# Optimization experiments

Hardware: AMD Instinct MI355X
Metric: run time of the kernel (lower is better)

The kernel has to match this reference:

```python
import jax, jax.numpy as jnp
import numpy as np

LATENT_SHAPES = [(192, 2, 2), (48, 4, 4), (24, 8, 8), (12, 16, 16), (6, 32, 32)]
B = 4          # batch
M = 32         # num_bases
HT, WT = 32, 32  # target spatial size = spatial size of z[-1] = (H/2, W/2)
EPS = 1e-3
CT = sum(s[0] for s in LATENT_SHAPES)  # 282


def _forward_fft(zs):
    # strided zero-insertion upsample of each latent to (HT, WT), concat channels, 2D FFT
    ups = []
    for zi in zs:
        b, c, h, w = zi.shape
        rh, rw = HT // h, WT // w
        u = jnp.zeros((b, c, HT, WT), zi.dtype).at[..., ::rh, ::rw].set(zi)
        ups.append(u)
    z = jnp.concatenate(ups, axis=1)            # (B, CT, HT, WT)
    return jnp.fft.fftn(z, axes=(-2, -1))       # complex64


def _inverse_fft(v_fft):
    # inverse FFT, take real part, split channels per level, strided downsample
    v = jnp.fft.ifftn(v_fft, axes=(-2, -1)).real  # (B, M, CT, HT, WT)
    splits = np.cumsum([s[0] for s in LATENT_SHAPES])[:-1]
    parts = jnp.split(v, splits, axis=-3)
    out = []
    for vi, (c, h, w) in zip(parts, LATENT_SHAPES):
        rh, rw = HT // h, WT // w
        out.append(vi[..., ::rh, ::rw])           # (B, M, c, h, w)
    return out


def _vector_field(zs, L, lam):
    z_fft = _forward_fft(zs)
    La = (L - jnp.swapaxes(L, -1, -2)).astype(jnp.complex64)        # antisymmetric (M, CT, CT)
    lam_a = (lam - jnp.roll(jnp.flip(lam, (1, 2)), (1, 1), axis=(1, 2))) * 1j  # (M, HT, WT) imaginary
    v_fft = jnp.einsum('mcd,bchw->bmdhw', La, z_fft)                 # (B, M, CT, HT, WT) complex
    v_fft = v_fft * lam_a[None, :, None, :, :]
    return _inverse_fft(v_fft)


def _log_prob(ws, zs, L, lam):
    S_ww = sum(jnp.einsum('bchw,bchw->b', wi, wi) for wi in ws)      # (B,)
    v = _vector_field(zs, L, lam)
    S_zz = sum(jnp.einsum('bnchw,bmchw->bnm', vi, vi) for vi in v)   # (B, M, M)
    S_zw = sum(jnp.einsum('bnchw,bchw->bn', vi, wi) for vi, wi in zip(v, ws))  # (B, M)
    var = jnp.maximum(jnp.mean(jnp.diagonal(S_zz, axis1=-2, axis2=-1), -1), 1e-6)
    std = jnp.sqrt(var)
    S_zz = S_zz / var[:, None, None]
    S_zw = S_zw / std[:, None]
    I = jnp.eye(M, dtype=S_zz.dtype)
    Mm = S_zz + EPS * I
    trace = EPS * S_ww + jnp.einsum('bn,bn->b', S_zw, S_zw)
    Lh = jnp.linalg.cholesky(Mm)
    logdet = 2.0 * jnp.sum(jnp.log(jnp.diagonal(Lh, axis1=-2, axis2=-1)), -1)
    return 0.5 * (logdet - trace)


def setup_inputs() -> dict:
    key = jax.random.key(0)
    ks = jax.random.split(key, 12)
    inp = {}
    for i, (c, h, w) in enumerate(LATENT_SHAPES):
        inp[f'z{i}'] = jax.random.normal(ks[i], (B, c, h, w), jnp.float32)
        inp[f'w{i}'] = jax.random.normal(ks[5 + i], (B, c, h, w), jnp.float32)
    inp['L'] = jax.random.normal(ks[10], (M, CT, CT), jnp.float32) * np.float32(1.0 / np.sqrt(CT))
    inp['lam'] = jax.random.normal(ks[11], (M, HT, WT), jnp.float32)
    return inp


def reference(z0, z1, z2, z3, z4, w0, w1, w2, w3, w4, L, lam):
    return _log_prob([w0, w1, w2, w3, w4], [z0, z1, z2, z3, z4], L, lam)
```

## Files before the change

kernel.cpp:

```cpp
#include <hip/hip_runtime.h>
#include <math.h>

#define NB 4
#define NM 32
#define CTOT 282
#define EPSV 1e-3f

__constant__ int g_cL[5]   = {192,48,24,12,6};
__constant__ int g_hL[5]   = {2,4,8,16,32};
__constant__ int g_coff[5] = {0,192,240,264,276};
__constant__ int g_zo[5]   = {0,768,1536,3072,6144};
__constant__ int g_po[4]   = {0,4,20,84};

__constant__ int t_lo[48] = {0,0,0,0,0,0,0,0,0,0,0,0,0,0,0,0,
                             0,0,0,0,0,0,0,0,0,0,0,0,0,0,0,0,
                             1,1,1,1,1,1,1,1, 2,2,2,2, 3,3, 4,4};
__constant__ int t_d0[48] = {0,6,12,18,24,30,36,42,48,54,60,66,72,78,84,90,
                             96,102,108,114,120,126,132,138,144,150,156,162,168,174,180,186,
                             192,198,204,210,216,222,228,234, 240,246,252,258, 264,270, 276,279};
__constant__ int t_nd[48] = {6,6,6,6,6,6,6,6,6,6,6,6,6,6,6,6,
                             6,6,6,6,6,6,6,6,6,6,6,6,6,6,6,6,
                             6,6,6,6,6,6,6,6, 6,6,6,6, 6,6, 3,3};

__constant__ int dft_l[30]  = {0,0,0, 1,1,1, 2,2,2,2,2,2,
                               3,3,3,3,3,3,3,3,3,3,3,3, 4,4,4,4,4,4};
__constant__ int dft_c0[30] = {0,64,128, 0,16,32, 0,4,8,12,16,20,
                               0,1,2,3,4,5,6,7,8,9,10,11, 0,1,2,3,4,5};
__constant__ int dft_nc[30] = {64,64,64, 16,16,16, 4,4,4,4,4,4,
                               1,1,1,1,1,1,1,1,1,1,1,1, 1,1,1,1,1,1};

#define N_LA     (NM*CTOT*CTOT)
#define OFF_LAT  0
#define OFF_ZRE  (OFF_LAT + N_LA)
#define OFF_ZIM  (OFF_ZRE + NB*12288)
#define OFF_WRE  (OFF_ZIM + NB*12288)
#define OFF_WIM  (OFF_WRE + NB*12288)
#define OFF_LAM  (OFF_WIM + NB*12288)
#define OFF_LAMF (OFF_LAM + NM*1024)
#define OFF_UR   (OFF_LAMF + NM*340)
#define OFF_UI   (OFF_UR + NB*NM*2720)
#define OFF_VRE  (OFF_UI + NB*NM*2720)
#define OFF_VIM  (OFF_VRE + NB*NM*12288)
#define OFF_SZZ  (OFF_VIM + NB*NM*12288)
#define OFF_SZW  (OFF_SZZ + NB*NM*NM)
#define OFF_SWW  (OFF_SZW + NB*NM)

#define PRE_LAT   (NM*81)
#define PRE_LAMF  (PRE_LAT + NM)
#define PRE_DFT   (PRE_LAMF + 2*NB*30)
#define PRE_SWW   (PRE_DFT + NB)
#define PRE_ZERO  (PRE_SWW + 17)

__global__ void __launch_bounds__(256) k_pre(
    const float* z0,const float* z1,const float* z2,const float* z3,const float* z4,
    const float* w0,const float* w1,const float* w2,const float* w3,const float* w4,
    const float* __restrict__ L, const float* __restrict__ lam, float* __restrict__ ws){
  __shared__ float shm[3136];
  int bid = blockIdx.x, t = threadIdx.x;
  if (bid < PRE_LAT){
    float* A  = shm;
    float* Bt = shm + 1056;
    int m = bid/81; int tl = bid%81;
    int d0 = (tl/9)*32, c0 = (tl%9)*32;
    const float* Lm = L + (size_t)m*CTOT*CTOT;
    for (int i=t;i<1024;i+=256){
      int r=i>>5, c=i&31;
      A[r*33+c]  = (c0+r<CTOT && d0+c<CTOT) ? Lm[(c0+r)*CTOT + d0+c] : 0.f;
      Bt[r*33+c] = (d0+r<CTOT && c0+c<CTOT) ? Lm[(d0+r)*CTOT + c0+c] : 0.f;
    }
    __syncthreads();
    float* out = ws + OFF_LAT + (size_t)m*CTOT*CTOT;
    for (int i=t;i<1024;i+=256){
      int r=i>>5, c=i&31;
      if (d0+r<CTOT && c0+c<CTOT)
        out[(size_t)(d0+r)*CTOT + c0+c] = A[c*33+r] - Bt[r*33+c];
    }
    return;
  }
  if (bid < PRE_LAMF){
    float* sA = shm;
    float* f3 = shm + 1024;
    float* f2 = shm + 1280;
    float* f1 = shm + 1344;
    int m = bid - PRE_LAT;
    for (int k=t;k<1024;k+=256){
      int ky=k>>5, kx=k&31;
      int nk = (((32-ky)&31)<<5) | ((32-kx)&31);
      float v = lam[(m<<10)+k] - lam[(m<<10)+nk];
      sA[k]=v;
      ws[OFF_LAM+(m<<10)+k]=v;
    }
    __syncthreads();
    { int s=t; int ky=s>>4, kx=s&15;
      float v = sA[(ky<<5)+kx]+sA[((ky+16)<<5)+kx]+sA[(ky<<5)+kx+16]+sA[((ky+16)<<5)+kx+16];
      f3[s]=v; ws[OFF_LAMF+m*340+84+s]=v; }
    __syncthreads();
    if (t<64){ int ky=t>>3, kx=t&7;
      float v = f3[(ky<<4)+kx]+f3[((ky+8)<<4)+kx]+f3[(ky<<4)+kx+8]+f3[((ky+8)<<4)+kx+8];
      f2[t]=v; ws[OFF_LAMF+m*340+20+t]=v; }
    __syncthreads();
    if (t<16){ int ky=t>>2, kx=t&3;
      float v = f2[(ky<<3)+kx]+f2[((ky+4)<<3)+kx]+f2[(ky<<3)+kx+4]+f2[((ky+4)<<3)+kx+4];
      f1[t]=v; ws[OFF_LAMF+m*340+4+t]=v; }
    __syncthreads();
    if (t<4){ int ky=t>>1, kx=t&1;
      float v = f1[(ky<<2)+kx]+f1[((ky+2)<<2)+kx]+f1[(ky<<2)+kx+2]+f1[((ky+2)<<2)+kx+2];
      ws[OFF_LAMF+m*340+t]=v; }
    return;
  }
  if (bid < PRE_DFT){
    float* sIn = shm;
    float* s1r = shm + 1024;
    float* s1i = shm + 2048;
    float* lc  = shm + 3072;
    float* lsn = shm + 3104;
    int i0 = bid - PRE_LAMF;
    int which = i0 / (NB*30);
    int rem = i0 % (NB*30);
    int b = rem / 30, j = rem % 30;
    int l = dft_l[j], c0 = dft_c0[j], nc = dft_nc[j];
    int h = g_hL[l], n = h*h;
    int elems = nc*n;
    const float* src;
    switch (which*5 + l){
      case 0: src=z0; break; case 1: src=z1; break; case 2: src=z2; break;
      case 3: src=z3; break; case 4: src=z4; break;
      case 5: src=w0; break; case 6: src=w1; break; case 7: src=w2; break;
      case 8: src=w3; break; default: src=w4; break;
    }
    for (int i=t;i<elems;i+=256) sIn[i] = src[(b*g_cL[l] + c0)*n + i];
    if (t<h){
      float ang = -6.2831853071795864f * (float)t / (float)h;
      lc[t] = cosf(ang); lsn[t] = sinf(ang);
    }
    __syncthreads();
    for (int p=t;p<elems;p+=256){
      int p2=p%n, cc=p/n;
      int y=p2/h, kx=p2-y*h;
      float re=0.f, im=0.f;
      for (int x=0;x<h;x++){
        int id = (kx*x)%h;
        float v = sIn[cc*n + y*h + x];
        re += v*lc[id]; im += v*lsn[id];
      }
      s1r[p]=re; s1i[p]=im;
    }
    __syncthreads();
    float scale = which ? 1.0f/(float)h : 1.0f;
    bool zt = (which==0 && l<4);
    float* outR = ws + (which?OFF_WRE:OFF_ZRE) + b*12288 + g_zo[l];
    float* outI = ws + (which?OFF_WIM:OFF_ZIM) + b*12288 + g_zo[l];
    for (int p=t;p<elems;p+=256){
      int p2=p%n, cc=p/n;
      int ky=p2/h, kx=p2-(p2/h)*h;
      float re=0.f, im=0.f;
      for (int y=0;y<h;y++){
        int id=(ky*y)%h;
        float c=lc[id], s=lsn[id];
        float ar=s1r[cc*n + y*h + kx], ai=s1i[cc*n + y*h + kx];
        re += ar*c - ai*s;
        im += ar*s + ai*c;
      }
      int o = zt ? (p2*g_cL[l] + c0 + cc) : ((c0+cc)*n + p2);
      outR[o]=re*scale; outI[o]=im*scale;
    }
    return;
  }
  if (bid < PRE_SWW){
    float* red = shm;
    int b = bid - PRE_DFT;
    const float* ptr[5] = {w0,w1,w2,w3,w4};
    float s = 0.f;
    for (int l=0;l<5;l++){
      int sz = g_cL[l]*g_hL[l]*g_hL[l];
      const float* p = ptr[l] + b*sz;
      for (int i=t;i<sz;i+=256){ float v=p[i]; s += v*v; }
    }
    red[t]=s; __syncthreads();
    for (int o=128;o>0;o>>=1){ if (t<o) red[t]+=red[t+o]; __syncthreads(); }
    if (t==0) ws[OFF_SWW + b] = red[0];
    return;
  }
  int i = (bid - PRE_SWW)*256 + t;
  if (i < NB*NM*NM + NB*NM) ws[OFF_SZZ + i] = 0.f;
}

__global__ void k_u(float* __restrict__ ws){
  __shared__ float pr[1024], pi[1024], q3r[256],q3i[256],q2r[64],q2i[64],q1r[16],q1i[16];
  int bid = blockIdx.x, t = threadIdx.x;
  int c = bid%6; int m = (bid/6)%NM; int b = bid/(6*NM);
  const float* la = ws+OFF_LAM+(m<<10);
  const float* zr = ws+OFF_ZRE+b*12288+6144+(c<<10);
  const float* zi = ws+OFF_ZIM+b*12288+6144+(c<<10);
  for (int k=t;k<1024;k+=256){ float f=la[k]; pr[k]=f*zr[k]; pi[k]=f*zi[k]; }
  __syncthreads();
  size_t base = (size_t)(b*NM+m)*2720;
  float* UR = ws+OFF_UR+base; float* UI = ws+OFF_UI+base;
  { int s=t; int ky=s>>4, kx=s&15;
    float r = pr[(ky<<5)+kx]+pr[((ky+16)<<5)+kx]+pr[(ky<<5)+kx+16]+pr[((ky+16)<<5)+kx+16];
    float ii= pi[(ky<<5)+kx]+pi[((ky+16)<<5)+kx]+pi[(ky<<5)+kx+16]+pi[((ky+16)<<5)+kx+16];
    q3r[s]=r; q3i[s]=ii; UR[(84+s)*8+c]=r; UI[(84+s)*8+c]=ii; }
  __syncthreads();
  if (t<64){ int ky=t>>3, kx=t&7;
    float r = q3r[(ky<<4)+kx]+q3r[((ky+8)<<4)+kx]+q3r[(ky<<4)+kx+8]+q3r[((ky+8)<<4)+kx+8];
    float ii= q3i[(ky<<4)+kx]+q3i[((ky+8)<<4)+kx]+q3i[(ky<<4)+kx+8]+q3i[((ky+8)<<4)+kx+8];
    q2r[t]=r; q2i[t]=ii; UR[(20+t)*8+c]=r; UI[(20+t)*8+c]=ii; }
  __syncthreads();
  if (t<16){ int ky=t>>2, kx=t&3;
    float r = q2r[(ky<<3)+kx]+q2r[((ky+4)<<3)+kx]+q2r[(ky<<3)+kx+4]+q2r[((ky+4)<<3)+kx+4];
    float ii= q2i[(ky<<3)+kx]+q2i[((ky+4)<<3)+kx]+q2i[(ky<<3)+kx+4]+q2i[((ky+4)<<3)+kx+4];
    q1r[t]=r; q1i[t]=ii; UR[(4+t)*8+c]=r; UI[(4+t)*8+c]=ii; }
  __syncthreads();
  if (t<4){ int ky=t>>1, kx=t&1;
    float r = q1r[(ky<<2)+kx]+q1r[((ky+2)<<2)+kx]+q1r[(ky<<2)+kx+2]+q1r[((ky+2)<<2)+kx+2];
    float ii= q1i[(ky<<2)+kx]+q1i[((ky+2)<<2)+kx]+q1i[(ky<<2)+kx+2]+q1i[((ky+2)<<2)+kx+2];
    UR[t*8+c]=r; UI[t*8+c]=ii; }
}

__global__ void __launch_bounds__(256) k_fold(float* __restrict__ ws){
  __shared__ float smem[6160];
  float* pre   = smem;
  float* pim   = smem + 2040;
  float* sLa   = smem + 4080;
  float* c64r  = smem + 4080;
  float* c64i  = smem + 4464;
  float* c16r  = smem + 4848;
  float* c16i  = smem + 4944;
  float* c4r   = smem + 5040;
  float* c4i   = smem + 5064;
  float* lamf  = smem + 5784;
  float* ssla  = smem + 6124;

  int t = threadIdx.x, bid = blockIdx.x;
  int m    = bid / (NB*48);
  int rem  = bid % (NB*48);
  int b    = rem / 48;
  int tile = rem % 48;
  int lo = t_lo[tile], d0 = t_d0[tile], nd = t_nd[tile];
  int ho = g_hL[lo];
  int nbins = ho*ho;
  const float* zreb = ws + OFF_ZRE + b*12288;
  const float* zimb = ws + OFF_ZIM + b*12288;
  const float* latm = ws + OFF_LAT + (size_t)m*CTOT*CTOT;

  for (int i=t;i<340;i+=256) lamf[i] = ws[OFF_LAMF + m*340 + i];
  for (int i=t;i<nd*282;i+=256){ int d=i/282, c=i-d*282; sLa[d*284+c] = latm[(size_t)(d0+d)*CTOT + c]; }
  if (t<nd*6){ int d=t/6, c=t-d*6; ssla[t] = latm[(size_t)(d0+d)*CTOT + 276 + c]; }

  int lA, kkA, c0A, offP; bool wrt;
  if (t<64){ lA=0; kkA=t&3; c0A=(t>>2)*12; offP=0; wrt=(t<4); }
  else if (t<128){ int i=t-64; lA=1; kkA=i&15; c0A=(i>>4)*12; offP=4; wrt=(i<16); }
  else { int i=t-128; lA=2; kkA=i>>1; c0A=(i&1)*12; offP=20; wrt=((i&1)==0); }
  float zAr[12], zAi[12], zBr[12], zBi[12];
  {
    int oA = g_zo[lA] + kkA*g_cL[lA] + c0A;
    const float4* zr4 = (const float4*)(zreb + oA);
    const float4* zi4 = (const float4*)(zimb + oA);
    float4 x0=zr4[0], x1=zr4[1], x2=zr4[2];
    float4 y0=zi4[0], y1=zi4[1], y2=zi4[2];
    zAr[0]=x0.x;zAr[1]=x0.y;zAr[2]=x0.z;zAr[3]=x0.w;zAr[4]=x1.x;zAr[5]=x1.y;zAr[6]=x1.z;zAr[7]=x1.w;zAr[8]=x2.x;zAr[9]=x2.y;zAr[10]=x2.z;zAr[11]=x2.w;
    zAi[0]=y0.x;zAi[1]=y0.y;zAi[2]=y0.z;zAi[3]=y0.w;zAi[4]=y1.x;zAi[5]=y1.y;zAi[6]=y1.z;zAi[7]=y1.w;zAi[8]=y2.x;zAi[9]=y2.y;zAi[10]=y2.z;zAi[11]=y2.w;
    int oB = 3072 + t*12;
    const float4* zr3 = (const float4*)(zreb + oB);
    const float4* zi3 = (const float4*)(zimb + oB);
    float4 p0=zr3[0], p1=zr3[1], p2=zr3[2];
    float4 q0=zi3[0], q1=zi3[1], q2=zi3[2];
    zBr[0]=p0.x;zBr[1]=p0.y;zBr[2]=p0.z;zBr[3]=p0.w;zBr[4]=p1.x;zBr[5]=p1.y;zBr[6]=p1.z;zBr[7]=p1.w;zBr[8]=p2.x;zBr[9]=p2.y;zBr[10]=p2.z;zBr[11]=p2.w;
    zBi[0]=q0.x;zBi[1]=q0.y;zBi[2]=q0.z;zBi[3]=q0.w;zBi[4]=q1.x;zBi[5]=q1.y;zBi[6]=q1.z;zBi[7]=q1.w;zBi[8]=q2.x;zBi[9]=q2.y;zBi[10]=q2.z;zBi[11]=q2.w;
  }
  __syncthreads();

  int offA = g_coff[lA] + c0A;
  for (int d=0; d<nd; d++){
    const float4* laA = (const float4*)(sLa + d*284 + offA);
    const float4* laB = (const float4*)(sLa + d*284 + 264);
    float4 a0=laA[0], a1=laA[1], a2=laA[2];
    float4 b0=laB[0], b1=laB[1], b2=laB[2];
    float av[12] = {a0.x,a0.y,a0.z,a0.w, a1.x,a1.y,a1.z,a1.w, a2.x,a2.y,a2.z,a2.w};
    float bv[12] = {b0.x,b0.y,b0.z,b0.w, b1.x,b1.y,b1.z,b1.w, b2.x,b2.y,b2.z,b2.w};
    float prA=0.f, piA=0.f, prB=0.f, piB=0.f;
    #pragma unroll
    for (int c=0;c<12;c++){ prA+=av[c]*zAr[c]; piA+=av[c]*zAi[c]; }
    #pragma unroll
    for (int c=0;c<12;c++){ prB+=bv[c]*zBr[c]; piB+=bv[c]*zBi[c]; }
    if (t<64){
      prA += __shfl_xor(prA, 4);  piA += __shfl_xor(piA, 4);
      prA += __shfl_xor(prA, 8);  piA += __shfl_xor(piA, 8);
      prA += __shfl_xor(prA,16);  piA += __shfl_xor(piA,16);
      prA += __shfl_xor(prA,32);  piA += __shfl_xor(piA,32);
    } else if (t<128){
      prA += __shfl_xor(prA,16);  piA += __shfl_xor(piA,16);
      prA += __shfl_xor(prA,32);  piA += __shfl_xor(piA,32);
    } else {
      prA += __shfl_xor(prA, 1);  piA += __shfl_xor(piA, 1);
    }
    if (wrt){ pre[d*340+offP+kkA]=prA; pim[d*340+offP+kkA]=piA; }
    pre[d*340+84+t]=prB; pim[d*340+84+t]=piB;
  }
  __syncthreads();

  float sc = (float)ho/1024.f;
  if (lo==4){
    int dlb = d0 - 276;
    const float* lamA = ws + OFF_LAM + (m<<10);
    float* vRb = ws + OFF_VRE + (size_t)(b*NM+m)*12288 + 6144 + (dlb<<10);
    float* vIb = ws + OFF_VIM + (size_t)(b*NM+m)*12288 + 6144 + (dlb<<10);
    const float* z4r = zreb + 6144;
    const float* z4i = zimb + 6144;
    for (int q=t; q<1024; q+=256){
      int ky=q>>5, kx=q&31;
      int a0=((ky&1)<<1)|(kx&1);
      int a1=4+(((ky&3)<<2)|(kx&3));
      int a2=20+(((ky&7)<<3)|(kx&7));
      int a3=84+(((ky&15)<<4)|(kx&15));
      float zr_[6], zi_[6];
      #pragma unroll
      for (int c=0;c<6;c++){ zr_[c]=z4r[(c<<10)+q]; zi_[c]=z4i[(c<<10)+q]; }
      float lm = lamA[q]*sc;
      for (int d=0; d<nd; d++){
        const float* pd = pre + d*340; const float* qd = pim + d*340;
        float Br = pd[a0]+pd[a1]+pd[a2]+pd[a3];
        float Bi = qd[a0]+qd[a1]+qd[a2]+qd[a3];
        #pragma unroll
        for (int c=0;c<6;c++){ float a=ssla[d*6+c]; Br+=a*zr_[c]; Bi+=a*zi_[c]; }
        vRb[(d<<10)+q] = -lm*Bi;
        vIb[(d<<10)+q] =  lm*Br;
      }
    }
    return;
  }

  if (lo<3){
    for (int idx=t; idx<nd*64; idx+=256){
      int d=idx>>6, k2=idx&63, ky=k2>>3, kx=k2&7;
      const float* pd = pre + d*340 + 84; const float* qd = pim + d*340 + 84;
      float r=0.f, ii=0.f;
      #pragma unroll
      for (int jy=0;jy<2;jy++)
        #pragma unroll
        for (int jx=0;jx<2;jx++){
          int a = ((ky+8*jy)<<4) | (kx+8*jx);
          float f = lamf[84+a];
          r += f*pd[a]; ii += f*qd[a];
        }
      if (lo<2){ float f=lamf[20+k2]; r+=f*pre[d*340+20+k2]; ii+=f*pim[d*340+20+k2]; }
      c64r[idx]=r; c64i[idx]=ii;
    }
  }
  __syncthreads();
  if (lo<2){
    for (int idx=t; idx<nd*16; idx+=256){
      int d=idx>>4, k2=idx&15, ky=k2>>2, kx=k2&3, base=d<<6;
      float r = c64r[base+(ky<<3)+kx]+c64r[base+((ky+4)<<3)+kx]+c64r[base+(ky<<3)+kx+4]+c64r[base+((ky+4)<<3)+kx+4];
      float ii= c64i[base+(ky<<3)+kx]+c64i[base+((ky+4)<<3)+kx]+c64i[base+(ky<<3)+kx+4]+c64i[base+((ky+4)<<3)+kx+4];
      if (lo<1){ float f=lamf[4+k2]; r+=f*pre[d*340+4+k2]; ii+=f*pim[d*340+4+k2]; }
      c16r[idx]=r; c16i[idx]=ii;
    }
  }
  __syncthreads();
  if (lo==0 && t<nd*4){
    int d=t>>2, k2=t&3, ky=k2>>1, kx=k2&1, base=d<<4;
    c4r[t]=c16r[base+(ky<<2)+kx]+c16r[base+((ky+2)<<2)+kx]+c16r[base+(ky<<2)+kx+2]+c16r[base+((ky+2)<<2)+kx+2];
    c4i[t]=c16i[base+(ky<<2)+kx]+c16i[base+((ky+2)<<2)+kx]+c16i[base+(ky<<2)+kx+2]+c16i[base+((ky+2)<<2)+kx+2];
  }
  __syncthreads();

  int dlb = d0 - g_coff[lo];
  float* vRb = ws + OFF_VRE + (size_t)(b*NM+m)*12288 + g_zo[lo];
  float* vIb = ws + OFF_VIM + (size_t)(b*NM+m)*12288 + g_zo[lo];
  const float* URg = ws + OFF_UR + (size_t)(b*NM+m)*2720;
  const float* UIg = ws + OFF_UI + (size_t)(b*NM+m)*2720;
  for (int idx=t; idx<nd*nbins; idx+=256){
    int d=idx/nbins, bin=idx-d*nbins;
    int ky=bin/ho, kx=bin-ky*ho;
    const float* pd = pre + d*340; const float* qd = pim + d*340;
    float Br = pd[((ky&1)<<1)|(kx&1)], Bi = qd[((ky&1)<<1)|(kx&1)];
    if (lo>=1){ int ix=4+(((ky&3)<<2)|(kx&3)); Br+=pd[ix]; Bi+=qd[ix]; }
    if (lo>=2){ int ix=20+(((ky&7)<<3)|(kx&7)); Br+=pd[ix]; Bi+=qd[ix]; }
    if (lo>=3){ int ix=84+(((ky&15)<<4)|(kx&15)); Br+=pd[ix]; Bi+=qd[ix]; }
    float lf = lamf[g_po[lo]+bin];
    float Vr = lf*Br, Vi = lf*Bi;
    if (lo==2){ Vr+=c64r[(d<<6)+bin]; Vi+=c64i[(d<<6)+bin]; }
    else if (lo==1){ Vr+=c16r[(d<<4)+bin]; Vi+=c16i[(d<<4)+bin]; }
    else if (lo==0){ Vr+=c4r[(d<<2)+bin]; Vi+=c4i[(d<<2)+bin]; }
    {
      int e = (g_po[lo]+bin)*8;
      const float4* ur4 = (const float4*)(URg + e);
      const float4* ui4 = (const float4*)(UIg + e);
      float4 u0=ur4[0], u1=ur4[1];
      float4 v0=ui4[0], v1=ui4[1];
      const float* sd = ssla + d*6;
      Vr += sd[0]*u0.x + sd[1]*u0.y + sd[2]*u0.z + sd[3]*u0.w + sd[4]*u1.x + sd[5]*u1.y;
      Vi += sd[0]*v0.x + sd[1]*v0.y + sd[2]*v0.z + sd[3]*v0.w + sd[4]*v1.x + sd[5]*v1.y;
    }
    int ob = (dlb+d)*nbins + bin;
    vRb[ob] = -sc*Vi;
    vIb[ob] =  sc*Vr;
  }
}

__global__ void __launch_bounds__(256) k_gram(float* __restrict__ ws){
  __shared__ float tile[32*132];
  __shared__ float wv[128];
  int t = threadIdx.x;
  int bid = blockIdx.x;
  int b = bid / 192, ch = bid % 192;
  int half = ch / 96;
  int k0 = (ch % 96) * 128;
  const float* V = ws + (half?OFF_VIM:OFF_VRE);
  const float* W = ws + (half?OFF_WIM:OFF_WRE) + b*12288 + k0;
  #pragma unroll
  for (int p=0;p<4;p++){
    int i4 = t + (p<<8);
    int row = i4 >> 5, c4 = i4 & 31;
    float4 v = *(const float4*)(V + (size_t)(b*NM+row)*12288 + k0 + (c4<<2));
    *(float4*)(tile + row*132 + (c4<<2)) = v;
  }
  if (t<128) wv[t] = W[t];
  __syncthreads();
  const float4* tf = (const float4*)tile;
  int n0 = t>>5, mm = t&31;
  float acc0=0.f, acc1=0.f, acc2=0.f, acc3=0.f;
  const float4* rm = tf + mm*33;
  const float4* r0 = tf + n0*33;
  const float4* r1 = tf + (n0+8)*33;
  const float4* r2 = tf + (n0+16)*33;
  const float4* r3 = tf + (n0+24)*33;
  for (int k4=0;k4<32;k4++){
    float4 vm = rm[k4];
    float4 v0 = r0[k4];
    float4 v1 = r1[k4];
    float4 v2 = r2[k4];
    float4 v3 = r3[k4];
    acc0 += v0.x*vm.x + v0.y*vm.y + v0.z*vm.z + v0.w*vm.w;
    acc1 += v1.x*vm.x + v1.y*vm.y + v1.z*vm.z + v1.w*vm.w;
    acc2 += v2.x*vm.x + v2.y*vm.y + v2.z*vm.z + v2.w*vm.w;
    acc3 += v3.x*vm.x + v3.y*vm.y + v3.z*vm.z + v3.w*vm.w;
  }
  float* szz = ws + OFF_SZZ + (b<<10);
  atomicAdd(&szz[(n0<<5) + mm], acc0);
  atomicAdd(&szz[((n0+8)<<5) + mm], acc1);
  atomicAdd(&szz[((n0+16)<<5) + mm], acc2);
  atomicAdd(&szz[((n0+24)<<5) + mm], acc3);
  if (t < 32){
    const float4* rn = tf + t*33;
    const float4* wf = (const float4*)wv;
    float acc=0.f;
    for (int k4=0;k4<32;k4++){
      float4 a = rn[k4]; float4 wq = wf[k4];
      acc += a.x*wq.x + a.y*wq.y + a.z*wq.z + a.w*wq.w;
    }
    atomicAdd(&ws[OFF_SZW + (b<<5) + t], acc);
  }
}

__global__ void k_final(float* __restrict__ ws, float* __restrict__ out){
  __shared__ float A[32][33];
  __shared__ float svar;
  int b = blockIdx.x, t = threadIdx.x;
  const float* szz = ws + OFF_SZZ + (b<<10);
  if (t==0){
    float s=0.f;
    for (int i=0;i<32;i++) s += szz[i*33];
    svar = fmaxf(s/32.0f, 1e-6f);
  }
  __syncthreads();
  float var = svar;
  for (int i=t;i<1024;i+=64){
    int r=i>>5, c=i&31;
    A[r][c] = szz[i]/var + ((r==c)?EPSV:0.0f);
  }
  __syncthreads();
  for (int j=0;j<32;j++){
    if (t==0) A[j][j] = sqrtf(A[j][j]);
    __syncthreads();
    if (t>j && t<32) A[t][j] /= A[j][j];
    __syncthreads();
    if (t>j && t<32){
      float lij = A[t][j];
      for (int k=j+1;k<=t;k++) A[t][k] -= lij*A[k][j];
    }
    __syncthreads();
  }
  if (t==0){
    float logdet=0.f;
    for (int j=0;j<32;j++) logdet += logf(A[j][j]);
    logdet *= 2.0f;
    const float* szw = ws + OFF_SZW + (b<<5);
    float s2=0.f;
    for (int n=0;n<32;n++) s2 += szw[n]*szw[n];
    float trace = EPSV*ws[OFF_SWW + b] + s2/var;
    out[b] = 0.5f*(logdet - trace);
  }
}

extern "C" void kernel_launch(void* const* d_in, const int* in_sizes, int n_in,
                              void* d_out, int out_size, void* d_ws, size_t ws_size,
                              hipStream_t stream){
  const float* z0 = (const float*)d_in[0];
  const float* w0 = (const float*)d_in[1];
  const float* z1 = (const float*)d_in[2];
  const float* w1 = (const float*)d_in[3];
  const float* z2 = (const float*)d_in[4];
  const float* w2 = (const float*)d_in[5];
  const float* z3 = (const float*)d_in[6];
  const float* w3 = (const float*)d_in[7];
  const float* z4 = (const float*)d_in[8];
  const float* w4 = (const float*)d_in[9];
  const float* L   = (const float*)d_in[10];
  const float* lam = (const float*)d_in[11];
  float* ws = (float*)d_ws;
  float* out = (float*)d_out;

  k_pre<<<PRE_ZERO, 256, 0, stream>>>(z0,z1,z2,z3,z4,w0,w1,w2,w3,w4, L, lam, ws);
  k_u<<<NB*NM*6, 256, 0, stream>>>(ws);
  k_fold<<<NB*NM*48, 256, 0, stream>>>(ws);
  k_gram<<<NB*192, 256, 0, stream>>>(ws);
  k_final<<<NB, 64, 0, stream>>>(ws, out);
}
```

Before: 208.5 us.

## Enlarge antisymmetrize tiles, pad DFT shared buffers, move z transpose into k_u

```diff
diff --git a/kernel.cpp b/kernel.cpp
--- a/kernel.cpp
+++ b/kernel.cpp
@@ -37,7 +37,9 @@
 #define OFF_WIM  (OFF_WRE + NB*12288)
 #define OFF_LAM  (OFF_WIM + NB*12288)
 #define OFF_LAMF (OFF_LAM + NM*1024)
-#define OFF_UR   (OFF_LAMF + NM*340)
+#define OFF_ZTR  (OFF_LAMF + NM*340)
+#define OFF_ZTI  (OFF_ZTR + NB*6144)
+#define OFF_UR   (OFF_ZTI + NB*6144)
 #define OFF_UI   (OFF_UR + NB*NM*2720)
 #define OFF_VRE  (OFF_UI + NB*NM*2720)
 #define OFF_VIM  (OFF_VRE + NB*NM*12288)
@@ -45,7 +47,7 @@
 #define OFF_SZW  (OFF_SZZ + NB*NM*NM)
 #define OFF_SWW  (OFF_SZW + NB*NM)
 
-#define PRE_LAT   (NM*81)
+#define PRE_LAT   (NM*25)
 #define PRE_LAMF  (PRE_LAT + NM)
 #define PRE_DFT   (PRE_LAMF + 2*NB*30)
 #define PRE_SWW   (PRE_DFT + NB)
@@ -55,25 +57,23 @@
     const float* z0,const float* z1,const float* z2,const float* z3,const float* z4,
     const float* w0,const float* w1,const float* w2,const float* w3,const float* w4,
     const float* __restrict__ L, const float* __restrict__ lam, float* __restrict__ ws){
-  __shared__ float shm[3136];
+  __shared__ float shm[4160];
   int bid = blockIdx.x, t = threadIdx.x;
   if (bid < PRE_LAT){
-    float* A  = shm;
-    float* Bt = shm + 1056;
-    int m = bid/81; int tl = bid%81;
-    int d0 = (tl/9)*32, c0 = (tl%9)*32;
+    int m = bid/25, tl = bid%25;
+    int d0 = (tl/5)*64, c0 = (tl%5)*64;
     const float* Lm = L + (size_t)m*CTOT*CTOT;
-    for (int i=t;i<1024;i+=256){
-      int r=i>>5, c=i&31;
-      A[r*33+c]  = (c0+r<CTOT && d0+c<CTOT) ? Lm[(c0+r)*CTOT + d0+c] : 0.f;
-      Bt[r*33+c] = (d0+r<CTOT && c0+c<CTOT) ? Lm[(d0+r)*CTOT + c0+c] : 0.f;
+    float* At = shm;
+    for (int i=t;i<4096;i+=256){
+      int r=i>>6, c=i&63;
+      At[r*65+c] = (c0+r<CTOT && d0+c<CTOT) ? Lm[(size_t)(c0+r)*CTOT + d0+c] : 0.f;
     }
     __syncthreads();
     float* out = ws + OFF_LAT + (size_t)m*CTOT*CTOT;
-    for (int i=t;i<1024;i+=256){
-      int r=i>>5, c=i&31;
+    for (int i=t;i<4096;i+=256){
+      int r=i>>6, c=i&63;
       if (d0+r<CTOT && c0+c<CTOT)
-        out[(size_t)(d0+r)*CTOT + c0+c] = A[c*33+r] - Bt[r*33+c];
+        out[(size_t)(d0+r)*CTOT + c0+c] = At[c*65+r] - Lm[(size_t)(d0+r)*CTOT + c0+c];
     }
     return;
   }
@@ -111,15 +111,17 @@
   if (bid < PRE_DFT){
     float* sIn = shm;
     float* s1r = shm + 1024;
-    float* s1i = shm + 2048;
-    float* lc  = shm + 3072;
-    float* lsn = shm + 3104;
+    float* s1i = shm + 2080;
+    float* lc  = shm + 3136;
+    float* lsn = shm + 3168;
     int i0 = bid - PRE_LAMF;
     int which = i0 / (NB*30);
     int rem = i0 % (NB*30);
     int b = rem / 30, j = rem % 30;
     int l = dft_l[j], c0 = dft_c0[j], nc = dft_nc[j];
     int h = g_hL[l], n = h*h;
+    int hp = h+1, n1 = h*hp;
+    int mult = 32/h;
     int elems = nc*n;
     const float* src;
     switch (which*5 + l){
@@ -129,8 +131,8 @@
       case 8: src=w3; break; default: src=w4; break;
     }
     for (int i=t;i<elems;i+=256) sIn[i] = src[(b*g_cL[l] + c0)*n + i];
-    if (t<h){
-      float ang = -6.2831853071795864f * (float)t / (float)h;
+    if (t<32){
+      float ang = -6.2831853071795864f * (float)t / 32.0f;
       lc[t] = cosf(ang); lsn[t] = sinf(ang);
     }
     __syncthreads();
@@ -139,30 +141,28 @@
       int y=p2/h, kx=p2-y*h;
       float re=0.f, im=0.f;
       for (int x=0;x<h;x++){
-        int id = (kx*x)%h;
+        int id = ((kx*x)%h)*mult;
         float v = sIn[cc*n + y*h + x];
         re += v*lc[id]; im += v*lsn[id];
       }
-      s1r[p]=re; s1i[p]=im;
+      s1r[cc*n1 + y*hp + kx]=re; s1i[cc*n1 + y*hp + kx]=im;
     }
     __syncthreads();
     float scale = which ? 1.0f/(float)h : 1.0f;
-    bool zt = (which==0 && l<4);
-    float* outR = ws + (which?OFF_WRE:OFF_ZRE) + b*12288 + g_zo[l];
-    float* outI = ws + (which?OFF_WIM:OFF_ZIM) + b*12288 + g_zo[l];
+    float* outR = ws + (which?OFF_WRE:OFF_ZRE) + b*12288 + g_zo[l] + c0*n;
+    float* outI = ws + (which?OFF_WIM:OFF_ZIM) + b*12288 + g_zo[l] + c0*n;
     for (int p=t;p<elems;p+=256){
       int p2=p%n, cc=p/n;
       int ky=p2/h, kx=p2-(p2/h)*h;
       float re=0.f, im=0.f;
       for (int y=0;y<h;y++){
-        int id=(ky*y)%h;
+        int id=((ky*y)%h)*mult;
         float c=lc[id], s=lsn[id];
-        float ar=s1r[cc*n + y*h + kx], ai=s1i[cc*n + y*h + kx];
+        float ar=s1r[cc*n1 + y*hp + kx], ai=s1i[cc*n1 + y*hp + kx];
         re += ar*c - ai*s;
         im += ar*s + ai*c;
       }
-      int o = zt ? (p2*g_cL[l] + c0 + cc) : ((c0+cc)*n + p2);
-      outR[o]=re*scale; outI[o]=im*scale;
+      outR[p]=re*scale; outI[p]=im*scale;
     }
     return;
   }
@@ -186,35 +186,60 @@
 }
 
 __global__ void k_u(float* __restrict__ ws){
-  __shared__ float pr[1024], pi[1024], q3r[256],q3i[256],q2r[64],q2i[64],q1r[16],q1i[16];
+  __shared__ float shm[6144];
   int bid = blockIdx.x, t = threadIdx.x;
-  int c = bid%6; int m = (bid/6)%NM; int b = bid/(6*NM);
-  const float* la = ws+OFF_LAM+(m<<10);
-  const float* zr = ws+OFF_ZRE+b*12288+6144+(c<<10);
-  const float* zi = ws+OFF_ZIM+b*12288+6144+(c<<10);
-  for (int k=t;k<1024;k+=256){ float f=la[k]; pr[k]=f*zr[k]; pi[k]=f*zi[k]; }
-  __syncthreads();
-  size_t base = (size_t)(b*NM+m)*2720;
-  float* UR = ws+OFF_UR+base; float* UI = ws+OFF_UI+base;
-  { int s=t; int ky=s>>4, kx=s&15;
-    float r = pr[(ky<<5)+kx]+pr[((ky+16)<<5)+kx]+pr[(ky<<5)+kx+16]+pr[((ky+16)<<5)+kx+16];
-    float ii= pi[(ky<<5)+kx]+pi[((ky+16)<<5)+kx]+pi[(ky<<5)+kx+16]+pi[((ky+16)<<5)+kx+16];
-    q3r[s]=r; q3i[s]=ii; UR[(84+s)*8+c]=r; UI[(84+s)*8+c]=ii; }
-  __syncthreads();
-  if (t<64){ int ky=t>>3, kx=t&7;
-    float r = q3r[(ky<<4)+kx]+q3r[((ky+8)<<4)+kx]+q3r[(ky<<4)+kx+8]+q3r[((ky+8)<<4)+kx+8];
-    float ii= q3i[(ky<<4)+kx]+q3i[((ky+8)<<4)+kx]+q3i[(ky<<4)+kx+8]+q3i[((ky+8)<<4)+kx+8];
-    q2r[t]=r; q2i[t]=ii; UR[(20+t)*8+c]=r; UI[(20+t)*8+c]=ii; }
-  __syncthreads();
-  if (t<16){ int ky=t>>2, kx=t&3;
-    float r = q2r[(ky<<3)+kx]+q2r[((ky+4)<<3)+kx]+q2r[(ky<<3)+kx+4]+q2r[((ky+4)<<3)+kx+4];
-    float ii= q2i[(ky<<3)+kx]+q2i[((ky+4)<<3)+kx]+q2i[(ky<<3)+kx+4]+q2i[((ky+4)<<3)+kx+4];
-    q1r[t]=r; q1i[t]=ii; UR[(4+t)*8+c]=r; UI[(4+t)*8+c]=ii; }
-  __syncthreads();
-  if (t<4){ int ky=t>>1, kx=t&1;
-    float r = q1r[(ky<<2)+kx]+q1r[((ky+2)<<2)+kx]+q1r[(ky<<2)+kx+2]+q1r[((ky+2)<<2)+kx+2];
-    float ii= q1i[(ky<<2)+kx]+q1i[((ky+2)<<2)+kx]+q1i[(ky<<2)+kx+2]+q1i[((ky+2)<<2)+kx+2];
-    UR[t*8+c]=r; UI[t*8+c]=ii; }
+  if (bid < NB*NM*6){
+    float* pr = shm;
+    float* pi = shm + 1024;
+    float* q3r= shm + 2048;
+    float* q3i= shm + 2304;
+    float* q2r= shm + 2560;
+    float* q2i= shm + 2624;
+    float* q1r= shm + 2688;
+    float* q1i= shm + 2704;
+    int c = bid%6; int m = (bid/6)%NM; int b = bid/(6*NM);
+    const float* la = ws+OFF_LAM+(m<<10);
+    const float* zr = ws+OFF_ZRE+b*12288+6144+(c<<10);
+    const float* zi = ws+OFF_ZIM+b*12288+6144+(c<<10);
+    for (int k=t;k<1024;k+=256){ float f=la[k]; pr[k]=f*zr[k]; pi[k]=f*zi[k]; }
+    __syncthreads();
+    size_t base = (size_t)(b*NM+m)*2720;
+    float* UR = ws+OFF_UR+base; float* UI = ws+OFF_UI+base;
+    { int s=t; int ky=s>>4, kx=s&15;
+      float r = pr[(ky<<5)+kx]+pr[((ky+16)<<5)+kx]+pr[(ky<<5)+kx+16]+pr[((ky+16)<<5)+kx+16];
+      float ii= pi[(ky<<5)+kx]+pi[((ky+16)<<5)+kx]+pi[(ky<<5)+kx+16]+pi[((ky+16)<<5)+kx+16];
+      q3r[s]=r; q3i[s]=ii; UR[(84+s)*8+c]=r; UI[(84+s)*8+c]=ii; }
+    __syncthreads();
+    if (t<64){ int ky=t>>3, kx=t&7;
+      float r = q3r[(ky<<4)+kx]+q3r[((ky+8)<<4)+kx]+q3r[(ky<<4)+kx+8]+q3r[((ky+8)<<4)+kx+8];
+      float ii= q3i[(ky<<4)+kx]+q3i[((ky+8)<<4)+kx]+q3i[(ky<<4)+kx+8]+q3i[((ky+8)<<4)+kx+8];
+      q2r[t]=r; q2i[t]=ii; UR[(20+t)*8+c]=r; UI[(20+t)*8+c]=ii; }
+    __syncthreads();
+    if (t<16){ int ky=t>>2, kx=t&3;
+      float r = q2r[(ky<<3)+kx]+q2r[((ky+4)<<3)+kx]+q2r[(ky<<3)+kx+4]+q2r[((ky+4)<<3)+kx+4];
+      float ii= q2i[(ky<<3)+kx]+q2i[((ky+4)<<3)+kx]+q2i[(ky<<3)+kx+4]+q2i[((ky+4)<<3)+kx+4];
+      q1r[t]=r; q1i[t]=ii; UR[(4+t)*8+c]=r; UI[(4+t)*8+c]=ii; }
+    __syncthreads();
+    if (t<4){ int ky=t>>1, kx=t&1;
+      float r = q1r[(ky<<2)+kx]+q1r[((ky+2)<<2)+kx]+q1r[(ky<<2)+kx+2]+q1r[((ky+2)<<2)+kx+2];
+      float ii= q1i[(ky<<2)+kx]+q1i[((ky+2)<<2)+kx]+q1i[(ky<<2)+kx+2]+q1i[((ky+2)<<2)+kx+2];
+      UR[t*8+c]=r; UI[t*8+c]=ii; }
+    return;
+  }
+  int tid = bid - NB*NM*6;
+  int b = tid>>1, ri = tid&1;
+  const float* src = ws + (ri?OFF_ZIM:OFF_ZRE) + b*12288;
+  float* dst = ws + (ri?OFF_ZTI:OFF_ZTR) + b*6144;
+  for (int i=t;i<6144;i+=256) shm[i]=src[i];
+  __syncthreads();
+  for (int q=t;q<6144;q+=256){
+    int s;
+    if (q<768){ int bin=q/192, c=q-bin*192; s=c*4+bin; }
+    else if (q<1536){ int q2=q-768; int bin=q2/48, c=q2-bin*48; s=768+c*16+bin; }
+    else if (q<3072){ int q2=q-1536; int bin=q2/24, c=q2-bin*24; s=1536+c*64+bin; }
+    else { int q2=q-3072; int bin=q2/12, c=q2-bin*12; s=3072+c*256+bin; }
+    dst[q]=shm[s];
+  }
 }
 
 __global__ void __launch_bounds__(256) k_fold(float* __restrict__ ws){
@@ -241,6 +266,8 @@
   int nbins = ho*ho;
   const float* zreb = ws + OFF_ZRE + b*12288;
   const float* zimb = ws + OFF_ZIM + b*12288;
+  const float* ztr  = ws + OFF_ZTR + b*6144;
+  const float* zti  = ws + OFF_ZTI + b*6144;
   const float* latm = ws + OFF_LAT + (size_t)m*CTOT*CTOT;
 
   for (int i=t;i<340;i+=256) lamf[i] = ws[OFF_LAMF + m*340 + i];
@@ -254,15 +281,15 @@
   float zAr[12], zAi[12], zBr[12], zBi[12];
   {
     int oA = g_zo[lA] + kkA*g_cL[lA] + c0A;
-    const float4* zr4 = (const float4*)(zreb + oA);
-    const float4* zi4 = (const float4*)(zimb + oA);
+    const float4* zr4 = (const float4*)(ztr + oA);
+    const float4* zi4 = (const float4*)(zti + oA);
     float4 x0=zr4[0], x1=zr4[1], x2=zr4[2];
     float4 y0=zi4[0], y1=zi4[1], y2=zi4[2];
     zAr[0]=x0.x;zAr[1]=x0.y;zAr[2]=x0.z;zAr[3]=x0.w;zAr[4]=x1.x;zAr[5]=x1.y;zAr[6]=x1.z;zAr[7]=x1.w;zAr[8]=x2.x;zAr[9]=x2.y;zAr[10]=x2.z;zAr[11]=x2.w;
     zAi[0]=y0.x;zAi[1]=y0.y;zAi[2]=y0.z;zAi[3]=y0.w;zAi[4]=y1.x;zAi[5]=y1.y;zAi[6]=y1.z;zAi[7]=y1.w;zAi[8]=y2.x;zAi[9]=y2.y;zAi[10]=y2.z;zAi[11]=y2.w;
     int oB = 3072 + t*12;
-    const float4* zr3 = (const float4*)(zreb + oB);
-    const float4* zi3 = (const float4*)(zimb + oB);
+    const float4* zr3 = (const float4*)(ztr + oB);
+    const float4* zi3 = (const float4*)(zti + oB);
     float4 p0=zr3[0], p1=zr3[1], p2=zr3[2];
     float4 q0=zi3[0], q1=zi3[1], q2=zi3[2];
     zBr[0]=p0.x;zBr[1]=p0.y;zBr[2]=p0.z;zBr[3]=p0.w;zBr[4]=p1.x;zBr[5]=p1.y;zBr[6]=p1.z;zBr[7]=p1.w;zBr[8]=p2.x;zBr[9]=p2.y;zBr[10]=p2.z;zBr[11]=p2.w;
@@ -513,7 +540,7 @@
   float* out = (float*)d_out;
 
   k_pre<<<PRE_ZERO, 256, 0, stream>>>(z0,z1,z2,z3,z4,w0,w1,w2,w3,w4, L, lam, ws);
-  k_u<<<NB*NM*6, 256, 0, stream>>>(ws);
+  k_u<<<NB*NM*6 + NB*2, 256, 0, stream>>>(ws);
   k_fold<<<NB*NM*48, 256, 0, stream>>>(ws);
   k_gram<<<NB*192, 256, 0, stream>>>(ws);
   k_final<<<NB, 64, 0, stream>>>(ws, out);
```

Result: faster. 201.3 us (-3.4%).
